# Optimization experiments

Hardware: AMD Instinct MI355X
Metric: run time of the kernel (lower is better)

The kernel has to match this reference:

```python
import jax, jax.numpy as jnp
import numpy as np

BATCH, T, S, M = 512, 4096, 64, 125  # batch, seq_len, n_states, emission alphabet (5^3)


def setup_inputs() -> dict:
    key = jax.random.key(0)
    k1, k2, k3, k4 = jax.random.split(key, 4)
    obs = jax.random.randint(k1, (BATCH, T), 0, M)
    x = jax.nn.one_hot(obs, M, dtype=jnp.float32)            # [B, T, M] one-hot emissions
    I = jax.nn.softmax(jax.random.normal(k2, (1, S)))        # initial state distribution [1, S]
    A = jax.nn.softmax(jax.random.normal(k3, (S, S)), axis=-1)   # transition matrix, rows sum to 1
    Bm = jax.nn.softmax(jax.random.normal(k4, (M, S)), axis=0)   # emission matrix, cols sum to 1
    return {"x": x, "I": I, "A": A, "Bm": Bm}


def reference(x, I, A, Bm):
    """HMM forward algorithm with per-step normalization (default scaling branch of CgpHmmCell).

    Returns the accumulated log-likelihood [B, 1].
    """
    xT = jnp.swapaxes(x, 0, 1)  # [T, B, M] for scan over time

    # t = 1: R = I (broadcast over batch), old_loglik = 0
    E0 = xT[0] @ Bm                                  # [B, S]
    u0 = E0 * I                                      # unscaled alpha
    Z0 = jnp.sum(u0, axis=1, keepdims=True)          # [B, 1]
    carry0 = (u0 / Z0, jnp.log(Z0))

    def step(carry, x_t):
        alpha, ll = carry
        R = alpha @ A                                # [B, S] transition
        E = x_t @ Bm                                 # [B, S] emission lookup (one-hot matmul)
        u = E * R
        Z = jnp.sum(u, axis=1, keepdims=True)        # per-sequence scaling factor
        return (u / Z, ll + jnp.log(Z)), None

    (alpha, loglik), _ = jax.lax.scan(step, carry0, xT[1:])
    return loglik
```

## Files before the change

### kernel.cpp

```cpp
#include <hip/hip_runtime.h>


#define BATCH 512
#define T 4096
#define S 64
#define M 125
#define CHUNKP 4
#define BURNP 2
#define NPACK 6
#define WPB 4
#define NQ 4

typedef __attribute__((ext_vector_type(8))) short bf16x8;
typedef __attribute__((ext_vector_type(4))) float f32x4;

union BFU { unsigned u[4]; bf16x8 v; };

__device__ __forceinline__ unsigned pk_trunc(float a, float b) {
    return (__float_as_uint(b) & 0xFFFF0000u) | (__float_as_uint(a) >> 16);
}
__device__ __forceinline__ unsigned pk_rne(float a, float b) {
    unsigned ua = __float_as_uint(a); ua += 0x7FFFu + ((ua >> 16) & 1u);
    unsigned ub = __float_as_uint(b); ub += 0x7FFFu + ((ub >> 16) & 1u);
    return (ub & 0xFFFF0000u) | (ua >> 16);
}

__global__ __launch_bounds__(256) void extract_obs(const float4* __restrict__ x4,
                                                   unsigned char* __restrict__ obs) {
    const long long n4 = (long long)BATCH * T * M / 4;
    long long stride = (long long)gridDim.x * blockDim.x;
    for (long long i = (long long)blockIdx.x * blockDim.x + threadIdx.x; i < n4; i += stride) {
        float4 v = x4[i];
        if (v.x != 0.0f || v.y != 0.0f || v.z != 0.0f || v.w != 0.0f) {
            long long e = i * 4;
            if (v.x != 0.0f) { long long r = (e + 0) / M; obs[r] = (unsigned char)(e + 0 - r * M); }
            if (v.y != 0.0f) { long long r = (e + 1) / M; obs[r] = (unsigned char)(e + 1 - r * M); }
            if (v.z != 0.0f) { long long r = (e + 2) / M; obs[r] = (unsigned char)(e + 2 - r * M); }
            if (v.w != 0.0f) { long long r = (e + 3) / M; obs[r] = (unsigned char)(e + 3 - r * M); }
        }
    }
}

__global__ __launch_bounds__(256) void hmm_mfma(const unsigned char* __restrict__ obs,
                                                const float* __restrict__ Iv,
                                                const float* __restrict__ A,
                                                const float* __restrict__ Bm,
                                                float* __restrict__ out) {
    __shared__ __align__(16) float BmL[M * S];
    __shared__ __align__(16) float ILds[S];

    const int tid = threadIdx.x, lane = tid & 63;
    const int s = lane & 15, g = lane >> 4;

    for (int i = tid; i < M * S; i += WPB * 64) BmL[i] = Bm[i];
    if (tid < S) ILds[tid] = Iv[tid];
    __syncthreads();

    BFU Af[4][2];
#pragma unroll
    for (int mt = 0; mt < 4; ++mt)
#pragma unroll
        for (int kf = 0; kf < 2; ++kf)
#pragma unroll
            for (int j2 = 0; j2 < 4; ++j2) {
                int p0 = 32 * kf + 16 * (j2 >> 1) + 4 * g + 2 * (j2 & 1);
                Af[mt][kf].u[j2] = pk_rne(A[(size_t)p0 * S + mt * 16 + s],
                                          A[(size_t)(p0 + 1) * S + mt * 16 + s]);
            }

    const int W = blockIdx.x * WPB + (tid >> 6);
    const int seq = W >> 1, half = W & 1;
    const unsigned long long* orow = (const unsigned long long*)(obs + (size_t)seq * T);
    const int adrC = s << 2;

    int idx0[NQ];
    unsigned long long u[NQ], un[NQ];
    BFU Bf[NQ][2];
    float Ls[NQ], S0v[NQ], cc[NQ], swv[NQ];
#pragma unroll
    for (int q = 0; q < NQ; ++q) {
        int chunk = half * 64 + q * 16 + s;
        idx0[q] = chunk * CHUNKP - BURNP;
        u[q] = orow[idx0[q] < 0 ? 0 : idx0[q]];
        Ls[q] = 0.f; S0v[q] = 0.f; cc[q] = 1.f; swv[q] = 1.f;
#pragma unroll
        for (int kf = 0; kf < 2; ++kf)
#pragma unroll
            for (int j = 0; j < 4; ++j) Bf[q][kf].u[j] = 0x3F803F80u;
    }

    for (int p = 0; p < NPACK; ++p) {
#pragma unroll
        for (int q = 0; q < NQ; ++q) {
            int in_ = idx0[q] + p + 1;
            in_ = in_ < 0 ? 0 : (in_ > T / 8 - 1 ? T / 8 - 1 : in_);
            un[q] = orow[in_];
        }
        const bool ovp = (half == 0) && (p == BURNP);
#pragma unroll
        for (int k = 0; k < 8; ++k) {
            f32x4 E[NQ][4];
#pragma unroll
            for (int q = 0; q < NQ; ++q) {
                const int o = (int)((u[q] >> (8 * k)) & 255ull);
                const float* br = &BmL[o << 6];
#pragma unroll
                for (int mt = 0; mt < 4; ++mt)
                    E[q][mt] = *(const f32x4*)&br[mt * 16 + g * 4];
            }
#pragma unroll
            for (int q = 0; q < NQ; ++q) {
                float w[4][4];
#pragma unroll
                for (int mt = 0; mt < 4; ++mt) {
                    f32x4 z = {0.f, 0.f, 0.f, 0.f};
                    z = __builtin_amdgcn_mfma_f32_16x16x32_bf16(Af[mt][0].v, Bf[q][0].v, z, 0, 0, 0);
                    z = __builtin_amdgcn_mfma_f32_16x16x32_bf16(Af[mt][1].v, Bf[q][1].v, z, 0, 0, 0);
#pragma unroll
                    for (int r = 0; r < 4; ++r) w[mt][r] = z[r] * E[q][mt][r];
                }
                if (ovp && k == 0 && q == 0) {
                    const bool c0 = (s == 0);
#pragma unroll
                    for (int mt = 0; mt < 4; ++mt)
#pragma unroll
                        for (int r = 0; r < 4; ++r)
                            w[mt][r] = c0 ? ILds[mt * 16 + g * 4 + r] * E[q][mt][r] : w[mt][r];
                }
                float scale = 1.f;
                if (k == 7) {
                    float swl = 0.f;
#pragma unroll
                    for (int mt = 0; mt < 4; ++mt)
#pragma unroll
                        for (int r = 0; r < 4; ++r) swl += w[mt][r];
                    swl += __shfl_xor(swl, 16);
                    swl += __shfl_xor(swl, 32);
                    swv[q] = swl;
                    float c = __uint_as_float(__builtin_amdgcn_ds_bpermute(adrC, __float_as_uint(w[0][0])));
                    c = fmaxf(c, 1e-37f);
                    cc[q] = c;
                    Ls[q] += __log2f(c);
                    scale = __builtin_amdgcn_rcpf(c);
                }
#pragma unroll
                for (int kf = 0; kf < 2; ++kf)
#pragma unroll
                    for (int j2 = 0; j2 < 4; ++j2) {
                        int mt = 2 * kf + (j2 >> 1), pr = j2 & 1;
                        float v0 = w[mt][2 * pr], v1 = w[mt][2 * pr + 1];
                        if (k == 7) { v0 *= scale; v1 *= scale; }
                        Bf[q][kf].u[j2] = pk_trunc(v0, v1);
                    }
            }
        }
        if (p == BURNP - 1) {
#pragma unroll
            for (int q = 0; q < NQ; ++q) {
                const bool ch0 = (half == 0) && (q == 0) && (s == 0);
                S0v[q] = ch0 ? Ls[q] : (Ls[q] + __log2f(swv[q]) - __log2f(cc[q]));
            }
        }
#pragma unroll
        for (int q = 0; q < NQ; ++q) u[q] = un[q];
    }

    float tot = 0.f;
#pragma unroll
    for (int q = 0; q < NQ; ++q)
        tot += Ls[q] + __log2f(swv[q]) - __log2f(cc[q]) - S0v[q];
    tot += __shfl_xor(tot, 1);
    tot += __shfl_xor(tot, 2);
    tot += __shfl_xor(tot, 4);
    tot += __shfl_xor(tot, 8);
    if (lane == 0)
        atomicAdd(out + seq, tot * 0.6931471805599453f);
}

extern "C" void kernel_launch(void* const* d_in, const int* in_sizes, int n_in,
                              void* d_out, int out_size, void* d_ws, size_t ws_size,
                              hipStream_t stream) {
    const float* x  = (const float*)d_in[0];
    const float* I  = (const float*)d_in[1];
    const float* A  = (const float*)d_in[2];
    const float* Bm = (const float*)d_in[3];
    float* out = (float*)d_out;
    unsigned char* obs = (unsigned char*)d_ws;

    hipMemsetAsync(out, 0, (size_t)out_size * sizeof(float), stream);
    extract_obs<<<65536, 256, 0, stream>>>((const float4*)x, obs);
    hmm_mfma<<<256, WPB * 64, 0, stream>>>(obs, I, A, Bm, out);
}
```

Measured before the change: 1.322 ms.

## Scan one-hot rows per thread with early exit; interleave emission loads with MFMA

The observation extraction kernel now gives each thread one row of 125 floats, scans it in 16-element groups and stops at the first group holding a nonzero, instead of streaming every float4 of the tensor. This is meant to skip reading most of the large one-hot tensor, since on average only part of each row is touched. The cost is uncoalesced strided per-thread loads, each thread walking its own 500-byte row. Separately, the emission-row loads in the HMM kernel are moved inside the per-sequence loop to cut register pressure, at the risk of less load latency hiding.

```diff
diff --git a/kernel.cpp b/kernel.cpp
--- a/kernel.cpp
+++ b/kernel.cpp
@@ -25,20 +25,26 @@
     return (ub & 0xFFFF0000u) | (ua >> 16);
 }
 
-__global__ __launch_bounds__(256) void extract_obs(const float4* __restrict__ x4,
+__global__ __launch_bounds__(256) void extract_obs(const float* __restrict__ x,
                                                    unsigned char* __restrict__ obs) {
-    const long long n4 = (long long)BATCH * T * M / 4;
-    long long stride = (long long)gridDim.x * blockDim.x;
-    for (long long i = (long long)blockIdx.x * blockDim.x + threadIdx.x; i < n4; i += stride) {
-        float4 v = x4[i];
-        if (v.x != 0.0f || v.y != 0.0f || v.z != 0.0f || v.w != 0.0f) {
-            long long e = i * 4;
-            if (v.x != 0.0f) { long long r = (e + 0) / M; obs[r] = (unsigned char)(e + 0 - r * M); }
-            if (v.y != 0.0f) { long long r = (e + 1) / M; obs[r] = (unsigned char)(e + 1 - r * M); }
-            if (v.z != 0.0f) { long long r = (e + 2) / M; obs[r] = (unsigned char)(e + 2 - r * M); }
-            if (v.w != 0.0f) { long long r = (e + 3) / M; obs[r] = (unsigned char)(e + 3 - r * M); }
-        }
+    const long long row = (long long)blockIdx.x * 256 + threadIdx.x;
+    const float* r = x + row * (long long)M;
+    int o = 0;
+#pragma unroll 1
+    for (int j = 0; j < 8; ++j) {
+        const int base = j * 16;
+        const int n = (j < 7) ? 16 : (M - 112);
+        float v[16];
+#pragma unroll
+        for (int t = 0; t < 16; ++t)
+            v[t] = (t < n) ? r[base + t] : 0.0f;
+        int found = -1;
+#pragma unroll
+        for (int t = 0; t < 16; ++t)
+            if (v[t] != 0.0f) found = base + t;
+        if (found >= 0) { o = found; break; }
     }
+    obs[row] = (unsigned char)o;
 }
 
 __global__ __launch_bounds__(256) void hmm_mfma(const unsigned char* __restrict__ obs,
@@ -99,17 +105,14 @@
         const bool ovp = (half == 0) && (p == BURNP);
 #pragma unroll
         for (int k = 0; k < 8; ++k) {
-            f32x4 E[NQ][4];
 #pragma unroll
             for (int q = 0; q < NQ; ++q) {
                 const int o = (int)((u[q] >> (8 * k)) & 255ull);
                 const float* br = &BmL[o << 6];
+                f32x4 E[4];
 #pragma unroll
                 for (int mt = 0; mt < 4; ++mt)
-                    E[q][mt] = *(const f32x4*)&br[mt * 16 + g * 4];
-            }
-#pragma unroll
-            for (int q = 0; q < NQ; ++q) {
+                    E[mt] = *(const f32x4*)&br[mt * 16 + g * 4];
                 float w[4][4];
 #pragma unroll
                 for (int mt = 0; mt < 4; ++mt) {
@@ -117,7 +120,7 @@
                     z = __builtin_amdgcn_mfma_f32_16x16x32_bf16(Af[mt][0].v, Bf[q][0].v, z, 0, 0, 0);
                     z = __builtin_amdgcn_mfma_f32_16x16x32_bf16(Af[mt][1].v, Bf[q][1].v, z, 0, 0, 0);
 #pragma unroll
-                    for (int r = 0; r < 4; ++r) w[mt][r] = z[r] * E[q][mt][r];
+                    for (int r = 0; r < 4; ++r) w[mt][r] = z[r] * E[mt][r];
                 }
                 if (ovp && k == 0 && q == 0) {
                     const bool c0 = (s == 0);
@@ -125,7 +128,7 @@
                     for (int mt = 0; mt < 4; ++mt)
 #pragma unroll
                         for (int r = 0; r < 4; ++r)
-                            w[mt][r] = c0 ? ILds[mt * 16 + g * 4 + r] * E[q][mt][r] : w[mt][r];
+                            w[mt][r] = c0 ? ILds[mt * 16 + g * 4 + r] * E[mt][r] : w[mt][r];
                 }
                 float scale = 1.f;
                 if (k == 7) {
@@ -188,6 +191,6 @@
     unsigned char* obs = (unsigned char*)d_ws;
 
     hipMemsetAsync(out, 0, (size_t)out_size * sizeof(float), stream);
-    extract_obs<<<65536, 256, 0, stream>>>((const float4*)x, obs);
+    extract_obs<<<(BATCH * T) / 256, 256, 0, stream>>>(x, obs);
     hmm_mfma<<<256, WPB * 64, 0, stream>>>(obs, I, A, Bm, out);
 }
```

After: 1.480 ms. +11.9%, slower.
